# Kernel tuning notes

Hardware: AMD Instinct MI355X
Metric: run time of the kernel (lower is better)

## Reference

```python
import jax, jax.numpy as jnp
import numpy as np

M, K, N = 8192, 1024, 8192

def setup_inputs() -> dict:
    key = jax.random.key(0)
    k1, k2, k3, k4 = jax.random.split(key, 4)
    # a, b are int8-valued quantized tensors (stored as int32 per harness dtype set)
    a = jax.random.randint(k1, (M, K), 0, 127, dtype=jnp.int32)
    b = jax.random.randint(k2, (K, N), 0, 127, dtype=jnp.int32)
    alpha_row = jax.random.uniform(k3, (M, 1), dtype=jnp.float32)
    alpha_col = jax.random.uniform(k4, (1, N), dtype=jnp.float32)
    return {"a": a, "b": b, "alpha_row": alpha_row, "alpha_col": alpha_col}

def reference(a, b, alpha_row, alpha_col):
    # Faithful to TorchGemmA8W8.forward: upcast int8 operands to fp32,
    # matmul with fp32 accumulate, cast result to int8.
    # (alpha_row / alpha_col are accepted but unused in this variant.)
    x = jnp.matmul(a.astype(jnp.float32), b.astype(jnp.float32))  # [M, N] fp32
    return x.astype(jnp.int8)
```

## Files before the change

kernel.cpp:

```cpp
#include <hip/hip_runtime.h>
#include <stdint.h>

#define M_DIM 8192
#define N_DIM 8192
#define K_DIM 1024
#define BK    128

typedef int int4v __attribute__((ext_vector_type(4)));

__device__ __forceinline__ void gload16(const char* g, char* l) {
    __builtin_amdgcn_global_load_lds(
        (__attribute__((address_space(1))) void*)(void*)const_cast<char*>(g),
        (__attribute__((address_space(3))) void*)l,
        16, 0, 0);
}

__device__ __forceinline__ int sat8(int v) {
    v = v > 127 ? 127 : v;
    v = v < -128 ? -128 : v;
    return v;
}

__global__ __launch_bounds__(256) void pack_ab_kernel(const int* __restrict__ a,
                                                      const int* __restrict__ b,
                                                      int* __restrict__ outA,
                                                      char* __restrict__ outB) {
    __shared__ char tile[64][68];
    const int t = threadIdx.x;
    if (blockIdx.x < 8192) {
        int i = blockIdx.x * 256 + t;
        int4 v = ((const int4*)a)[i];
        outA[i] = (v.x & 0xff) | ((v.y & 0xff) << 8) |
                  ((v.z & 0xff) << 16) | ((v.w & 0xff) << 24);
        return;
    }
    const int bx = blockIdx.x - 8192;
    const int n0 = (bx & 127) * 64;
    const int k0 = (bx >> 7) * 64;
    const int tr  = t >> 4;
    const int tc4 = (t & 15) << 2;
#pragma unroll
    for (int j = 0; j < 4; ++j) {
        int row = tr + j * 16;
        int4 v = *(const int4*)&b[(size_t)(k0 + row) * N_DIM + n0 + tc4];
        tile[row][tc4 + 0] = (char)v.x;
        tile[row][tc4 + 1] = (char)v.y;
        tile[row][tc4 + 2] = (char)v.z;
        tile[row][tc4 + 3] = (char)v.w;
    }
    __syncthreads();
#pragma unroll
    for (int j = 0; j < 4; ++j) {
        int n = tr + j * 16;
        int pk = (tile[tc4 + 0][n] & 0xff) |
                 ((tile[tc4 + 1][n] & 0xff) << 8) |
                 ((tile[tc4 + 2][n] & 0xff) << 16) |
                 ((tile[tc4 + 3][n] & 0xff) << 24);
        *(int*)&outB[(size_t)(n0 + n) * K_DIM + k0 + tc4] = pk;
    }
}

__global__ __launch_bounds__(256) void gemm_i8_kernel(const char* __restrict__ A8,
                                                      const char* __restrict__ B8,
                                                      int* __restrict__ C) {
    __shared__ __align__(16) char smem[4 * 8704];
    char* As = smem;
    char* Bs = smem + 16384;

    const int t    = threadIdx.x;
    const int xcd  = blockIdx.x & 7;
    const int j    = blockIdx.x >> 3;
    const int bm   = (xcd << 3) | (j & 7);
    const int bn   = j >> 3;
    const int lane = t & 63;
    const int wave = t >> 6;
    const int wm   = wave >> 1;
    const int wn   = wave & 1;
    const int quad = lane >> 4;
    const int l16  = lane & 15;

    const size_t aBase = (size_t)(bm * 128) * K_DIM;
    const size_t bBase = (size_t)(bn * 128) * K_DIM;

    const int sr = t >> 2;
    const int swzc = (((t & 3) ^ ((t >> 3) & 3)) << 4);
    const int laneByte = ((quad ^ ((l16 >> 1) & 3)) << 4);

    int4v acc[4][4] = {};

    for (int kt = 0; kt < K_DIM / BK; ++kt) {
        const int kOff = kt * BK;
#pragma unroll
        for (int s = 0; s < 4; ++s) {
            const int p = s >> 1;
            const int rr = ((s & 1) << 6) + sr;
            const int f = s * 4096 + t * 16;
            gload16(A8 + aBase + (size_t)rr * K_DIM + kOff + p * 64 + swzc, As + f);
            gload16(B8 + bBase + (size_t)rr * K_DIM + kOff + p * 64 + swzc, Bs + f);
        }
        __syncthreads();

#pragma unroll
        for (int h = 0; h < 2; ++h) {
            int4v af[4], bf[4];
#pragma unroll
            for (int mi = 0; mi < 4; ++mi)
                af[mi] = *(const int4v*)
                    &As[h * 8192 + (wm * 64 + mi * 16 + l16) * 64 + laneByte];
#pragma unroll
            for (int ni = 0; ni < 4; ++ni)
                bf[ni] = *(const int4v*)
                    &Bs[h * 8192 + (wn * 64 + ni * 16 + l16) * 64 + laneByte];

#pragma unroll
            for (int mi = 0; mi < 4; ++mi)
#pragma unroll
                for (int ni = 0; ni < 4; ++ni)
                    acc[mi][ni] = __builtin_amdgcn_mfma_i32_16x16x64_i8(
                        af[mi], bf[ni], acc[mi][ni], 0, 0, 0);
        }

        __syncthreads();
    }

    int* lw = (int*)(smem + wave * 8704);
    const int mW = bm * 128 + wm * 64;
    const int nW = bn * 128 + wn * 64;
#pragma unroll
    for (int rnd = 0; rnd < 2; ++rnd) {
#pragma unroll
        for (int mh = 0; mh < 2; ++mh) {
            const int mi = rnd * 2 + mh;
#pragma unroll
            for (int ni = 0; ni < 4; ++ni)
#pragma unroll
                for (int r = 0; r < 4; ++r)
                    lw[(mh * 16 + quad * 4 + r) * 68 + ni * 16 + l16] =
                        sat8(acc[mi][ni][r]);
        }
#pragma unroll
        for (int rr = 0; rr < 8; ++rr) {
            const int R = rr * 4 + quad;
            const int4v v = *(const int4v*)&lw[R * 68 + l16 * 4];
            *(int4v*)&C[(size_t)(mW + rnd * 32 + R) * N_DIM + nW + l16 * 4] = v;
        }
    }
}

__global__ __launch_bounds__(256) void gemm_naive_kernel(const int* __restrict__ a,
                                                         const int* __restrict__ b,
                                                         int* __restrict__ C) {
    const int col = blockIdx.x * 256 + threadIdx.x;
    const int row = blockIdx.y;
    int acc = 0;
    for (int k = 0; k < K_DIM; ++k)
        acc += a[(size_t)row * K_DIM + k] * b[(size_t)k * N_DIM + col];
    C[(size_t)row * N_DIM + col] = sat8(acc);
}

extern "C" void kernel_launch(void* const* d_in, const int* in_sizes, int n_in,
                              void* d_out, int out_size, void* d_ws, size_t ws_size,
                              hipStream_t stream) {
    const int* a = (const int*)d_in[0];
    const int* b = (const int*)d_in[1];
    int* out = (int*)d_out;

    const size_t needed = 2 * (size_t)M_DIM * K_DIM;
    if (ws_size < needed) {
        gemm_naive_kernel<<<dim3(N_DIM / 256, M_DIM), 256, 0, stream>>>(a, b, out);
        return;
    }

    char* A8 = (char*)d_ws;
    char* B8 = A8 + (size_t)M_DIM * K_DIM;

    pack_ab_kernel<<<8192 + 2048, 256, 0, stream>>>(a, b, (int*)A8, B8);
    gemm_i8_kernel<<<4096, 256, 0, stream>>>(A8, B8, out);
}
```

Before: 364.7 us.

## Load GEMM operands directly from global into registers, dropping LDS staging

Replaces the LDS-staged K loop, which used global_load_lds, barriers and shared-memory fragment reads, with per-wave direct global-to-register loads of A and B fragments. A two-stage register double buffer (a0/b0, a1/b1) prefetches the next K slice while MFMAs run on the current one, and the loop is fully unrolled. This removes LDS traffic and __syncthreads, at the cost of more global/L2 traffic: each wave now fetches its own fragments without sharing across waves, and loads are 16-byte strided rows that may coalesce poorly.

```diff
diff --git a/kernel.cpp b/kernel.cpp
--- a/kernel.cpp
+++ b/kernel.cpp
@@ -4,16 +4,8 @@
 #define M_DIM 8192
 #define N_DIM 8192
 #define K_DIM 1024
-#define BK    128
 
 typedef int int4v __attribute__((ext_vector_type(4)));
-
-__device__ __forceinline__ void gload16(const char* g, char* l) {
-    __builtin_amdgcn_global_load_lds(
-        (__attribute__((address_space(1))) void*)(void*)const_cast<char*>(g),
-        (__attribute__((address_space(3))) void*)l,
-        16, 0, 0);
-}
 
 __device__ __forceinline__ int sat8(int v) {
     v = v > 127 ? 127 : v;
@@ -64,8 +56,6 @@
                                                       const char* __restrict__ B8,
                                                       int* __restrict__ C) {
     __shared__ __align__(16) char smem[4 * 8704];
-    char* As = smem;
-    char* Bs = smem + 16384;
 
     const int t    = threadIdx.x;
     const int xcd  = blockIdx.x & 7;
@@ -79,48 +69,51 @@
     const int quad = lane >> 4;
     const int l16  = lane & 15;
 
-    const size_t aBase = (size_t)(bm * 128) * K_DIM;
-    const size_t bBase = (size_t)(bn * 128) * K_DIM;
-
-    const int sr = t >> 2;
-    const int swzc = (((t & 3) ^ ((t >> 3) & 3)) << 4);
-    const int laneByte = ((quad ^ ((l16 >> 1) & 3)) << 4);
+    const char* aW = A8 + ((size_t)(bm * 128 + wm * 64 + l16) << 10) + quad * 16;
+    const char* bW = B8 + ((size_t)(bn * 128 + wn * 64 + l16) << 10) + quad * 16;
 
     int4v acc[4][4] = {};
-
-    for (int kt = 0; kt < K_DIM / BK; ++kt) {
-        const int kOff = kt * BK;
-#pragma unroll
-        for (int s = 0; s < 4; ++s) {
-            const int p = s >> 1;
-            const int rr = ((s & 1) << 6) + sr;
-            const int f = s * 4096 + t * 16;
-            gload16(A8 + aBase + (size_t)rr * K_DIM + kOff + p * 64 + swzc, As + f);
-            gload16(B8 + bBase + (size_t)rr * K_DIM + kOff + p * 64 + swzc, Bs + f);
-        }
-        __syncthreads();
+    int4v a0[4], b0[4], a1[4], b1[4];
 
 #pragma unroll
-        for (int h = 0; h < 2; ++h) {
-            int4v af[4], bf[4];
+    for (int mi = 0; mi < 4; ++mi) {
+        a0[mi] = *(const int4v*)(aW + mi * 16384);
+        b0[mi] = *(const int4v*)(bW + mi * 16384);
+    }
 #pragma unroll
-            for (int mi = 0; mi < 4; ++mi)
-                af[mi] = *(const int4v*)
-                    &As[h * 8192 + (wm * 64 + mi * 16 + l16) * 64 + laneByte];
+    for (int mi = 0; mi < 4; ++mi) {
+        a1[mi] = *(const int4v*)(aW + mi * 16384 + 64);
+        b1[mi] = *(const int4v*)(bW + mi * 16384 + 64);
+    }
+
+#pragma unroll
+    for (int kt = 0; kt < 16; kt += 2) {
+#pragma unroll
+        for (int mi = 0; mi < 4; ++mi)
 #pragma unroll
             for (int ni = 0; ni < 4; ++ni)
-                bf[ni] = *(const int4v*)
-                    &Bs[h * 8192 + (wn * 64 + ni * 16 + l16) * 64 + laneByte];
-
+                acc[mi][ni] = __builtin_amdgcn_mfma_i32_16x16x64_i8(
+                    a0[mi], b0[ni], acc[mi][ni], 0, 0, 0);
+        if (kt + 2 < 16) {
 #pragma unroll
-            for (int mi = 0; mi < 4; ++mi)
+            for (int mi = 0; mi < 4; ++mi) {
+                a0[mi] = *(const int4v*)(aW + mi * 16384 + (kt + 2) * 64);
+                b0[mi] = *(const int4v*)(bW + mi * 16384 + (kt + 2) * 64);
+            }
+        }
 #pragma unroll
-                for (int ni = 0; ni < 4; ++ni)
-                    acc[mi][ni] = __builtin_amdgcn_mfma_i32_16x16x64_i8(
-                        af[mi], bf[ni], acc[mi][ni], 0, 0, 0);
+        for (int mi = 0; mi < 4; ++mi)
+#pragma unroll
+            for (int ni = 0; ni < 4; ++ni)
+                acc[mi][ni] = __builtin_amdgcn_mfma_i32_16x16x64_i8(
+                    a1[mi], b1[ni], acc[mi][ni], 0, 0, 0);
+        if (kt + 3 < 16) {
+#pragma unroll
+            for (int mi = 0; mi < 4; ++mi) {
+                a1[mi] = *(const int4v*)(aW + mi * 16384 + (kt + 3) * 64);
+                b1[mi] = *(const int4v*)(bW + mi * 16384 + (kt + 3) * 64);
+            }
         }
-
-        __syncthreads();
     }
 
     int* lw = (int*)(smem + wave * 8704);
```

After: 519.4 us. 42.4% more time.

## Pre-swizzle packed int8 operands into tile-contiguous layout for linear LDS loads

Applied to the files above, without the earlier changes.

The pack kernel now writes A and B in a blocked layout: each 128-row tile is stored as contiguous 64-byte-wide K slices, with the LDS XOR swizzle already applied. The GEMM main loop then loads each 16 KB tile chunk with fully linear global_load_lds addresses instead of strided per-row addresses. This is meant to improve global read coalescing and cut address arithmetic in the hot loop. In exchange, the pack kernel's stores become more scattered.

```diff
diff --git a/kernel.cpp b/kernel.cpp
--- a/kernel.cpp
+++ b/kernel.cpp
@@ -23,15 +23,22 @@
 
 __global__ __launch_bounds__(256) void pack_ab_kernel(const int* __restrict__ a,
                                                       const int* __restrict__ b,
-                                                      int* __restrict__ outA,
+                                                      char* __restrict__ outA,
                                                       char* __restrict__ outB) {
     __shared__ char tile[64][68];
     const int t = threadIdx.x;
     if (blockIdx.x < 8192) {
-        int i = blockIdx.x * 256 + t;
-        int4 v = ((const int4*)a)[i];
-        outA[i] = (v.x & 0xff) | ((v.y & 0xff) << 8) |
-                  ((v.z & 0xff) << 16) | ((v.w & 0xff) << 24);
+        const int m   = blockIdx.x;
+        const int row = m & 127;
+        const int xr  = (row >> 1) & 3;
+        const int4 v  = ((const int4*)a)[m * 256 + t];
+        const int pk  = (v.x & 0xff) | ((v.y & 0xff) << 8) |
+                        ((v.z & 0xff) << 16) | ((v.w & 0xff) << 24);
+        const int k     = t * 4;
+        const int slice = k >> 6;
+        const int sc    = ((k >> 4) & 3) ^ xr;
+        *(int*)&outA[(size_t)(m >> 7) * 131072 + slice * 8192 + row * 64 +
+                     sc * 16 + (k & 15)] = pk;
         return;
     }
     const int bx = blockIdx.x - 8192;
@@ -49,6 +56,7 @@
         tile[row][tc4 + 3] = (char)v.w;
     }
     __syncthreads();
+    const int slice = k0 >> 6;
 #pragma unroll
     for (int j = 0; j < 4; ++j) {
         int n = tr + j * 16;
@@ -56,7 +64,11 @@
                  ((tile[tc4 + 1][n] & 0xff) << 8) |
                  ((tile[tc4 + 2][n] & 0xff) << 16) |
                  ((tile[tc4 + 3][n] & 0xff) << 24);
-        *(int*)&outB[(size_t)(n0 + n) * K_DIM + k0 + tc4] = pk;
+        const int ng  = n0 + n;
+        const int row = ng & 127;
+        const int sc  = (tc4 >> 4) ^ ((row >> 1) & 3);
+        *(int*)&outB[(size_t)(ng >> 7) * 131072 + slice * 8192 + row * 64 +
+                     sc * 16 + (tc4 & 15)] = pk;
     }
 }
 
@@ -79,24 +91,20 @@
     const int quad = lane >> 4;
     const int l16  = lane & 15;
 
-    const size_t aBase = (size_t)(bm * 128) * K_DIM;
-    const size_t bBase = (size_t)(bn * 128) * K_DIM;
+    const char* aT = A8 + (size_t)bm * 131072;
+    const char* bT = B8 + (size_t)bn * 131072;
 
-    const int sr = t >> 2;
-    const int swzc = (((t & 3) ^ ((t >> 3) & 3)) << 4);
     const int laneByte = ((quad ^ ((l16 >> 1) & 3)) << 4);
 
     int4v acc[4][4] = {};
 
     for (int kt = 0; kt < K_DIM / BK; ++kt) {
-        const int kOff = kt * BK;
+        const size_t kBase = (size_t)kt * 16384;
 #pragma unroll
         for (int s = 0; s < 4; ++s) {
-            const int p = s >> 1;
-            const int rr = ((s & 1) << 6) + sr;
             const int f = s * 4096 + t * 16;
-            gload16(A8 + aBase + (size_t)rr * K_DIM + kOff + p * 64 + swzc, As + f);
-            gload16(B8 + bBase + (size_t)rr * K_DIM + kOff + p * 64 + swzc, Bs + f);
+            gload16(aT + kBase + f, As + f);
+            gload16(bT + kBase + f, Bs + f);
         }
         __syncthreads();
 
@@ -174,6 +182,6 @@
     char* A8 = (char*)d_ws;
     char* B8 = A8 + (size_t)M_DIM * K_DIM;
 
-    pack_ab_kernel<<<8192 + 2048, 256, 0, stream>>>(a, b, (int*)A8, B8);
+    pack_ab_kernel<<<8192 + 2048, 256, 0, stream>>>(a, b, A8, B8);
     gemm_i8_kernel<<<4096, 256, 0, stream>>>(A8, B8, out);
 }
```

Result: no change. 366.7 us (+0.5%).
